# Kernel optimization log

Hardware: AMD Instinct MI355X
Metric: run time of the kernel (lower is better)

Reference implementation:

```python
import jax, jax.numpy as jnp
import numpy as np

B, C, H, W = 8, 512, 56, 56
CI = C // 2  # inter_channels
EPS = 1e-5   # BatchNorm eps


def setup_inputs() -> dict:
    key = jax.random.key(0)
    ks = jax.random.split(key, 11)
    s = 0.02
    return {
        "x": jax.random.normal(ks[0], (B, C, H, W), jnp.float32),
        "theta_w": jax.random.normal(ks[1], (CI, C), jnp.float32) * s,
        "theta_b": jnp.zeros((CI,), jnp.float32),
        "phi_w": jax.random.normal(ks[2], (CI, C), jnp.float32) * s,
        "phi_b": jnp.zeros((CI,), jnp.float32),
        "g_w": jax.random.normal(ks[3], (CI, C), jnp.float32) * s,
        "g_b": jnp.zeros((CI,), jnp.float32),
        "w_w": jax.random.normal(ks[4], (C, CI), jnp.float32) * s,
        "w_b": jnp.zeros((C,), jnp.float32),
        "bn_gamma": jax.random.normal(ks[5], (C,), jnp.float32) * 0.1,
        "bn_beta": jax.random.normal(ks[6], (C,), jnp.float32) * 0.1,
    }


def reference(x, theta_w, theta_b, phi_w, phi_b, g_w, g_b, w_w, w_b, bn_gamma, bn_beta):
    b, c, h, w = x.shape
    n = h * w

    def proj(wt, bi):  # 1x1 conv -> [b, out, n]
        return (jnp.einsum('bchw,oc->bohw', x, wt) + bi[None, :, None, None]).reshape(b, -1, n)

    theta_x = proj(theta_w, theta_b).transpose(0, 2, 1)  # [b, n, ci]
    phi_x = proj(phi_w, phi_b)                           # [b, ci, n]
    g_x = proj(g_w, g_b).transpose(0, 2, 1)             # [b, n, ci]

    f = jnp.einsum('bnc,bcm->bnm', theta_x, phi_x)       # [b, n, n] unscaled scores
    f_div_c = jax.nn.softmax(f, axis=-1)
    y = jnp.einsum('bnm,bmc->bnc', f_div_c, g_x)         # [b, n, ci]
    y = y.transpose(0, 2, 1).reshape(b, -1, h, w)        # [b, ci, h, w]

    w_y = jnp.einsum('bchw,oc->bohw', y, w_w) + w_b[None, :, None, None]
    # BatchNorm2d (training mode, batch statistics over B,H,W per channel)
    mean = w_y.mean(axis=(0, 2, 3))
    var = w_y.var(axis=(0, 2, 3))
    w_y = (w_y - mean[None, :, None, None]) * jax.lax.rsqrt(var[None, :, None, None] + EPS)
    w_y = w_y * bn_gamma[None, :, None, None] + bn_beta[None, :, None, None]
    return w_y + x
```

## Files before the change

kernel.cpp:

```cpp
#include <hip/hip_runtime.h>
#include <hip/hip_bf16.h>


typedef unsigned short u16;
typedef unsigned int u32;
typedef __attribute__((ext_vector_type(8))) short short8;
typedef __attribute__((ext_vector_type(4))) float floatx4;

#define B_   8
#define C_   512
#define CI_  256
#define N_   3136
#define BN_  25088

__device__ __forceinline__ u16 f2b(float f) {
    return __builtin_bit_cast(u16, __float2bfloat16(f));
}
__device__ __forceinline__ float b2f(u16 u) {
    return __bfloat162float(__builtin_bit_cast(__hip_bfloat16, u));
}
__device__ __forceinline__ floatx4 mfma16(short8 a, short8 b, floatx4 c) {
    return __builtin_amdgcn_mfma_f32_16x16x32_bf16(a, b, c, 0, 0, 0);
}
__device__ __forceinline__ void gload_lds16(const u16* g, u16* l) {
    __builtin_amdgcn_global_load_lds(
        (const __attribute__((address_space(1))) u32*)g,
        (__attribute__((address_space(3))) u32*)l, 16, 0, 0);
}

__global__ void detect_dtype(const u32* __restrict__ xw, int* __restrict__ flag)
{
    __shared__ int cnt;
    if (threadIdx.x == 0) cnt = 0;
    __syncthreads();
    int c = 0;
    for (int i = 0; i < 16; ++i) {
        u32 w = xw[threadIdx.x * 16 + i];
        u32 e = (w >> 7) & 0xFF;
        c += (e >= 118 && e <= 130) ? 1 : 0;
    }
    atomicAdd(&cnt, c);
    __syncthreads();
    if (threadIdx.x == 0) *flag = (2 * cnt > 4096) ? 1 : 0;
}

__global__ __launch_bounds__(256) void convert_params(
    const void* tw, const void* tb, const void* pw, const void* pb,
    const void* gw, const void* gbi, const void* ww, const void* wb,
    const void* gamma, const void* beta,
    u16* __restrict__ dst, const int* __restrict__ flag)
{
    const void* srcs[10] = {tw, tb, pw, pb, gw, gbi, ww, wb, gamma, beta};
    const int ns[10] = {131072, 256, 131072, 256, 131072, 256, 131072, 512, 512, 512};
    int seg = blockIdx.y;
    int off = 0;
    for (int s = 0; s < 10; ++s) { if (s == seg) break; off += ns[s]; }
    const void* src = srcs[seg];
    int n = ns[seg];
    int i0 = (blockIdx.x * 256 + threadIdx.x) * 8;
    if (i0 >= n) return;
    const int fl = *flag;
    u16* d = dst + off;
    for (int k = 0; k < 8; ++k) {
        int i = i0 + k;
        if (i < n)
            d[i] = fl ? ((const u16*)src)[i] : f2b(((const float*)src)[i]);
    }
}

__global__ __launch_bounds__(256) void transpose_x(
    const void* __restrict__ in, u16* __restrict__ out,
    const int* __restrict__ flag)
{
    __shared__ u16 tile[64][68];
    const int fl = *flag;
    const int t = threadIdx.x;
    const long base = (long)blockIdx.z * (long)C_ * (long)N_;
    const int c0 = blockIdx.x * 64, r0 = blockIdx.y * 64;
    const int lr = t >> 3;
    const int lc = (t & 7) * 8;
#pragma unroll
    for (int j = 0; j < 2; ++j) {
        int rr = lr + 32 * j;
        long eoff = base + (long)(r0 + rr) * N_ + c0 + lc;
        u16 v[8] __attribute__((aligned(16)));
        if (fl) {
            const u16* pi = (const u16*)in + eoff;
            *(uint64_t*)&v[0] = *(const uint64_t*)pi;
            *(uint64_t*)&v[4] = *(const uint64_t*)(pi + 4);
        } else {
            const float* pi = (const float*)in + eoff;
            floatx4 a = *(const floatx4*)pi;
            floatx4 b4 = *(const floatx4*)(pi + 4);
#pragma unroll
            for (int k = 0; k < 4; ++k) { v[k] = f2b(a[k]); v[4 + k] = f2b(b4[k]); }
        }
        *(uint64_t*)&tile[rr][lc] = *(const uint64_t*)&v[0];
        *(uint64_t*)&tile[rr][lc + 4] = *(const uint64_t*)&v[4];
    }
    __syncthreads();
#pragma unroll
    for (int j = 0; j < 2; ++j) {
        int oc = lr + 32 * j;
        int ob = (t & 7) * 8;
        u16 vals[8] __attribute__((aligned(16)));
#pragma unroll
        for (int k = 0; k < 8; ++k) vals[k] = tile[ob + k][oc];
        u16* po = out + (long)blockIdx.z * N_ * C_ + (long)(c0 + oc) * C_ + r0 + ob;
        *(uint64_t*)po = *(const uint64_t*)vals;
        *(uint64_t*)(po + 4) = *(const uint64_t*)(vals + 4);
    }
}

__global__ __launch_bounds__(256) void transpose64(
    const u16* __restrict__ in, u16* __restrict__ out, int R, int Cc)
{
    __shared__ u16 tile[64][68];
    const int t = threadIdx.x;
    const long base = (long)blockIdx.z * (long)R * (long)Cc;
    const int c0 = blockIdx.x * 64, r0 = blockIdx.y * 64;
    const int lr = t >> 3;
    const int lc = (t & 7) * 8;
#pragma unroll
    for (int j = 0; j < 2; ++j) {
        int rr = lr + 32 * j;
        const u16* pi = in + base + (long)(r0 + rr) * Cc + c0 + lc;
        *(uint64_t*)&tile[rr][lc] = *(const uint64_t*)pi;
        *(uint64_t*)&tile[rr][lc + 4] = *(const uint64_t*)(pi + 4);
    }
    __syncthreads();
#pragma unroll
    for (int j = 0; j < 2; ++j) {
        int oc = lr + 32 * j;
        int ob = (t & 7) * 8;
        u16 vals[8] __attribute__((aligned(16)));
#pragma unroll
        for (int k = 0; k < 8; ++k) vals[k] = tile[ob + k][oc];
        u16* po = out + base + (long)(c0 + oc) * R + r0 + ob;
        *(uint64_t*)po = *(const uint64_t*)vals;
        *(uint64_t*)(po + 4) = *(const uint64_t*)(vals + 4);
    }
}

template<int K>
__global__ __launch_bounds__(256) void gemm_bt(
    const u16* __restrict__ A, long a_bstride,
    const u16* __restrict__ Bt,
    const u16* __restrict__ bias,
    u16* __restrict__ Out, long out_bstride,
    int ncols)
{
    const int t = threadIdx.x;
    const int wave = t >> 6, lane = t & 63;
    const int q = lane >> 4, lx = lane & 15;
    const int m0 = blockIdx.x * 64;
    const int n0c = blockIdx.y * 64;
    const int b = blockIdx.z;
    const u16* Ab = A + (long)b * a_bstride;

    __shared__ u16 As[64][40];
    __shared__ u16 Bs[64][40];

    floatx4 zero4 = {0.f, 0.f, 0.f, 0.f};
    floatx4 acc[2][2];
#pragma unroll
    for (int i = 0; i < 2; ++i)
#pragma unroll
        for (int j = 0; j < 2; ++j) acc[i][j] = zero4;

    const int sr = t >> 2;
    const int sc = (t & 3) * 8;
    const int wr = (wave >> 1) * 32;
    const int wc = (wave & 1) * 32;

    for (int k0 = 0; k0 < K; k0 += 32) {
        *(short8*)&As[sr][sc] =
            *(const short8*)(Ab + (long)(m0 + sr) * K + k0 + sc);
        *(short8*)&Bs[sr][sc] =
            *(const short8*)(Bt + (long)(n0c + sr) * K + k0 + sc);
        __syncthreads();
        short8 af[2], bfr[2];
#pragma unroll
        for (int i = 0; i < 2; ++i)
            af[i] = *(const short8*)&As[wr + 16 * i + lx][q * 8];
#pragma unroll
        for (int j = 0; j < 2; ++j)
            bfr[j] = *(const short8*)&Bs[wc + 16 * j + lx][q * 8];
#pragma unroll
        for (int i = 0; i < 2; ++i)
#pragma unroll
            for (int j = 0; j < 2; ++j)
                acc[i][j] = mfma16(af[i], bfr[j], acc[i][j]);
        __syncthreads();
    }

#pragma unroll
    for (int i = 0; i < 2; ++i) {
#pragma unroll
        for (int j = 0; j < 2; ++j) {
            int col = n0c + wc + 16 * j + lx;
            float bv = b2f(bias[col]);
#pragma unroll
            for (int r = 0; r < 4; ++r) {
                int row = m0 + wr + 16 * i + q * 4 + r;
                Out[(long)b * out_bstride + (long)row * ncols + col] =
                    f2b(acc[i][j][r] + bv);
            }
        }
    }
}

__global__ __launch_bounds__(256, 2) void attn(
    const u16* __restrict__ theta,
    const u16* __restrict__ phi,
    const u16* __restrict__ gT,
    u16* __restrict__ ypart,
    float* __restrict__ lpart)
{
    __shared__ u16 ps[2][8][32][32];
    __shared__ u16 gs[2][256][32];
    __shared__ u16 Ps[4][32][40];

    const int t = threadIdx.x;
    const int wave = t >> 6, lane = t & 63;
    const int q = lane >> 4, lx = lane & 15;
    const int b = blockIdx.y;
    const int z = blockIdx.z;
    const int n0w = blockIdx.x * 128 + wave * 32;
    const bool valid = n0w < N_;
    const u16* thb = theta + (long)b * N_ * CI_;
    const u16* phb = phi + (long)b * N_ * CI_;
    const u16* gb = gT + (long)b * CI_ * N_;

    short8 tf[2][8];
#pragma unroll
    for (int h = 0; h < 2; ++h) {
        int trow = n0w + h * 16 + lx;
        if (trow >= N_) trow = N_ - 1;
#pragma unroll
        for (int kk = 0; kk < 8; ++kk)
            tf[h][kk] = *(const short8*)(thb + (long)trow * CI_ + kk * 32 + q * 8);
    }

    floatx4 zero4 = {0.f, 0.f, 0.f, 0.f};
    floatx4 yacc[2][16];
#pragma unroll
    for (int h = 0; h < 2; ++h)
#pragma unroll
        for (int i = 0; i < 16; ++i) yacc[h][i] = zero4;
    floatx4 lacc[2] = {zero4, zero4};
    const short8 ones = {0x3F80, 0x3F80, 0x3F80, 0x3F80,
                         0x3F80, 0x3F80, 0x3F80, 0x3F80};

    const int mbeg = z * (N_ / 2);
    const int lrow = lane >> 2;
    const int lcol = (lane & 3) * 8;

    auto stage = [&](int buf, int m0) {
#pragma unroll
        for (int i = 0; i < 2; ++i) {
            int kc = wave * 2 + i;
#pragma unroll
            for (int h = 0; h < 2; ++h)
                gload_lds16(phb + (long)(m0 + h * 16 + lrow) * CI_ + kc * 32 + lcol,
                            &ps[buf][kc][h * 16][0]);
        }
#pragma unroll
        for (int j4 = 0; j4 < 4; ++j4) {
            int j = wave * 4 + j4;
            gload_lds16(gb + (long)(j * 16 + lrow) * N_ + m0 + lcol,
                        &gs[buf][j * 16][0]);
        }
    };

    stage(0, mbeg);
    const int NSTEP = (N_ / 2) / 32;
    for (int s = 0; s < NSTEP; ++s) {
        const int buf = s & 1;
        __syncthreads();
        if (s + 1 < NSTEP) stage(buf ^ 1, mbeg + (s + 1) * 32);

        floatx4 sacc[2][2];
        sacc[0][0] = zero4; sacc[0][1] = zero4;
        sacc[1][0] = zero4; sacc[1][1] = zero4;
#pragma unroll
        for (int kk = 0; kk < 8; ++kk) {
            short8 bf0 = *(const short8*)&ps[buf][kk][lx][q * 8];
            short8 bf1 = *(const short8*)&ps[buf][kk][16 + lx][q * 8];
            sacc[0][0] = mfma16(tf[0][kk], bf0, sacc[0][0]);
            sacc[1][0] = mfma16(tf[1][kk], bf0, sacc[1][0]);
            sacc[0][1] = mfma16(tf[0][kk], bf1, sacc[0][1]);
            sacc[1][1] = mfma16(tf[1][kk], bf1, sacc[1][1]);
        }

#pragma unroll
        for (int h = 0; h < 2; ++h)
#pragma unroll
            for (int mh = 0; mh < 2; ++mh)
#pragma unroll
                for (int r = 0; r < 4; ++r) {
                    float e = __expf(fminf(sacc[h][mh][r], 60.f));
                    Ps[wave][h * 16 + q * 4 + r][mh * 16 + lx] = f2b(e);
                }
        __builtin_amdgcn_wave_barrier();
        short8 pA0 = *(const short8*)&Ps[wave][lx][q * 8];
        short8 pA1 = *(const short8*)&Ps[wave][16 + lx][q * 8];
        __builtin_amdgcn_wave_barrier();

#pragma unroll
        for (int ct = 0; ct < 16; ++ct) {
            short8 gf = *(const short8*)&gs[buf][ct * 16 + lx][q * 8];
            yacc[0][ct] = mfma16(pA0, gf, yacc[0][ct]);
            yacc[1][ct] = mfma16(pA1, gf, yacc[1][ct]);
        }
        lacc[0] = mfma16(pA0, ones, lacc[0]);
        lacc[1] = mfma16(pA1, ones, lacc[1]);
    }

    if (valid) {
        u16* yb = ypart + (long)z * B_ * N_ * CI_ + (long)b * N_ * CI_;
#pragma unroll
        for (int h = 0; h < 2; ++h)
#pragma unroll
            for (int ct = 0; ct < 16; ++ct)
#pragma unroll
                for (int r = 0; r < 4; ++r)
                    yb[(long)(n0w + h * 16 + q * 4 + r) * CI_ + ct * 16 + lx] =
                        f2b(yacc[h][ct][r]);
        if (lx == 0) {
#pragma unroll
            for (int h = 0; h < 2; ++h)
#pragma unroll
                for (int r = 0; r < 4; ++r)
                    lpart[(long)z * BN_ + (long)b * N_ + n0w + h * 16 + q * 4 + r] =
                        lacc[h][r];
        }
    }
}

__global__ __launch_bounds__(256) void attn_combine(
    const u16* __restrict__ ypart, const float* __restrict__ lpart,
    u16* __restrict__ y)
{
    long tt = (long)blockIdx.x * 256 + threadIdx.x;
    long row = tt >> 5;
    int cb = (int)(tt & 31) * 8;
    float l = lpart[row] + lpart[BN_ + row];
    float rl = 1.0f / l;
    const u16* p0 = ypart + row * CI_ + cb;
    const u16* p1 = p0 + (long)B_ * N_ * CI_;
    short8 v0 = *(const short8*)p0;
    short8 v1 = *(const short8*)p1;
    u16 ov[8] __attribute__((aligned(16)));
#pragma unroll
    for (int j = 0; j < 8; ++j)
        ov[j] = f2b((b2f(((const u16*)&v0)[j]) + b2f(((const u16*)&v1)[j])) * rl);
    *(short8*)(y + row * CI_ + cb) = *(const short8*)ov;
}

__global__ void zero_stats(float* stats) {
    stats[threadIdx.x] = 0.f;
    stats[threadIdx.x + 256] = 0.f;
    stats[threadIdx.x + 512] = 0.f;
    stats[threadIdx.x + 768] = 0.f;
}

__global__ __launch_bounds__(256) void bn_stats(
    const u16* __restrict__ wy, float* __restrict__ stats)
{
    const int t = threadIdx.x;
    const long row0 = (long)blockIdx.x * 256;
    float s0 = 0.f, s1 = 0.f, q0 = 0.f, q1 = 0.f;
    for (int r = 0; r < 256; ++r) {
        const u16* p = wy + (row0 + r) * C_;
        float a = b2f(p[t]), b = b2f(p[t + 256]);
        s0 += a; q0 += a * a;
        s1 += b; q1 += b * b;
    }
    atomicAdd(&stats[t], s0);
    atomicAdd(&stats[t + 256], s1);
    atomicAdd(&stats[C_ + t], q0);
    atomicAdd(&stats[C_ + t + 256], q1);
}

__global__ __launch_bounds__(256) void bn_apply(
    const u16* __restrict__ wy, const void* __restrict__ xv,
    const u16* __restrict__ gamma, const u16* __restrict__ beta,
    const float* __restrict__ stats, void* __restrict__ outv,
    const int* __restrict__ flag)
{
    __shared__ float tile[64][65];
    const int fl = *flag;
    const int t = threadIdx.x;
    const int nb0 = blockIdx.x * 64;
    const int c0 = blockIdx.y * 64;
    const int b = blockIdx.z;
#pragma unroll
    for (int j = 0; j < 4; ++j) {
        int row = (t >> 4) + 16 * j;
        int col = (t & 15) * 4;
        const u16* p = wy + ((long)b * N_ + nb0 + row) * C_ + c0 + col;
        u16 lv[4] __attribute__((aligned(8)));
        *(uint64_t*)lv = *(const uint64_t*)p;
#pragma unroll
        for (int k = 0; k < 4; ++k) tile[row][col + k] = b2f(lv[k]);
    }
    __syncthreads();
    const float inv = 1.0f / (float)BN_;
#pragma unroll
    for (int it = 0; it < 8; ++it) {
        int oc = (t >> 5) + 8 * it;
        int on = (t & 31) * 2;
        int c = c0 + oc;
        float mean = stats[c] * inv;
        float var = stats[C_ + c] * inv - mean * mean;
        float rstd = rsqrtf(var + 1e-5f);
        float sc = b2f(gamma[c]) * rstd;
        float sh = b2f(beta[c]) - mean * sc;
        long base = ((long)b * C_ + c) * N_ + nb0 + on;
        float v0 = tile[on][oc] * sc + sh;
        float v1 = tile[on + 1][oc] * sc + sh;
        if (fl) {
            v0 += b2f(((const u16*)xv)[base]);
            v1 += b2f(((const u16*)xv)[base + 1]);
            ((u16*)outv)[base] = f2b(v0);
            ((u16*)outv)[base + 1] = f2b(v1);
        } else {
            v0 += ((const float*)xv)[base];
            v1 += ((const float*)xv)[base + 1];
            ((float*)outv)[base] = v0;
            ((float*)outv)[base + 1] = v1;
        }
    }
}

extern "C" void kernel_launch(void* const* d_in, const int* in_sizes, int n_in,
                              void* d_out, int out_size, void* d_ws, size_t ws_size,
                              hipStream_t stream)
{
    (void)in_sizes; (void)n_in; (void)out_size; (void)ws_size;

    const size_t S = 12845056;
    char* base = (char*)d_ws;
    u16*   xT    = (u16*)(base);
    u16*   gT    = (u16*)(base);
    u16*   y     = (u16*)(base + S);
    u16*   th    = (u16*)(base + 2 * S);
    u16*   ph    = (u16*)(base + 3 * S);
    u16*   wy    = (u16*)(base + 2 * S);
    u16*   gn    = (u16*)(base + 4 * S);
    float* lpart = (float*)(base + 5 * S);
    float* stats = (float*)(base + 5 * S + (size_t)2 * BN_ * 4);
    u16*   cw    = (u16*)(base + 5 * S + (size_t)2 * BN_ * 4 + 4096);
    int*   flag  = (int*)(base + 5 * S + (size_t)2 * BN_ * 4 + 4096 + 1055744);

    u16* ctw = cw;               u16* ctb = cw + 131072;
    u16* cpw = ctb + 256;        u16* cpb = cpw + 131072;
    u16* cgw = cpb + 256;        u16* cgb = cgw + 131072;
    u16* cww = cgb + 256;        u16* cwb = cww + 131072;
    u16* cga = cwb + 512;        u16* cbe = cga + 512;

    u16* ypart = (u16*)d_out;

    detect_dtype<<<1, 256, 0, stream>>>((const u32*)d_in[0], flag);
    convert_params<<<dim3(64, 10), 256, 0, stream>>>(
        d_in[1], d_in[2], d_in[3], d_in[4], d_in[5], d_in[6], d_in[7],
        d_in[8], d_in[9], d_in[10], cw, flag);

    transpose_x<<<dim3(N_ / 64, C_ / 64, B_), 256, 0, stream>>>(d_in[0], xT, flag);

    gemm_bt<C_><<<dim3(N_ / 64, CI_ / 64, B_), 256, 0, stream>>>(
        xT, (long)N_ * C_, ctw, ctb, th, (long)N_ * CI_, CI_);
    gemm_bt<C_><<<dim3(N_ / 64, CI_ / 64, B_), 256, 0, stream>>>(
        xT, (long)N_ * C_, cpw, cpb, ph, (long)N_ * CI_, CI_);
    gemm_bt<C_><<<dim3(N_ / 64, CI_ / 64, B_), 256, 0, stream>>>(
        xT, (long)N_ * C_, cgw, cgb, gn, (long)N_ * CI_, CI_);

    transpose64<<<dim3(CI_ / 64, N_ / 64, B_), 256, 0, stream>>>(gn, gT, N_, CI_);

    attn<<<dim3(25, B_, 2), 256, 0, stream>>>(th, ph, gT, ypart, lpart);

    attn_combine<<<dim3((BN_ * 32) / 256), 256, 0, stream>>>(ypart, lpart, y);

    gemm_bt<CI_><<<dim3(N_ / 64, C_ / 64, B_), 256, 0, stream>>>(
        y, (long)N_ * CI_, cww, cwb, wy, (long)N_ * C_, C_);

    zero_stats<<<1, 256, 0, stream>>>(stats);
    bn_stats<<<BN_ / 256, 256, 0, stream>>>(wy, stats);

    bn_apply<<<dim3(N_ / 64, C_ / 64, B_), 256, 0, stream>>>(
        wy, d_in[0], cga, cbe, stats, d_out, flag);
}
```

Before: 392.0 us.

## Use fragment-ordered LDS layouts and double-buffered async loads in GEMM and attention

Measured after the change: 428.8 us. 1.09x slower.

```diff
diff --git a/kernel.cpp b/kernel.cpp
--- a/kernel.cpp
+++ b/kernel.cpp
@@ -143,13 +143,16 @@
 }
 
 template<int K>
-__global__ __launch_bounds__(256) void gemm_bt(
+__global__ __launch_bounds__(256, 4) void gemm_bt(
     const u16* __restrict__ A, long a_bstride,
     const u16* __restrict__ Bt,
     const u16* __restrict__ bias,
     u16* __restrict__ Out, long out_bstride,
     int ncols)
 {
+    __shared__ __attribute__((aligned(16))) u16 Asf[2][2][4][64][8];
+    __shared__ __attribute__((aligned(16))) u16 Bsf[2][2][4][64][8];
+
     const int t = threadIdx.x;
     const int wave = t >> 6, lane = t & 63;
     const int q = lane >> 4, lx = lane & 15;
@@ -158,9 +161,6 @@
     const int b = blockIdx.z;
     const u16* Ab = A + (long)b * a_bstride;
 
-    __shared__ u16 As[64][40];
-    __shared__ u16 Bs[64][40];
-
     floatx4 zero4 = {0.f, 0.f, 0.f, 0.f};
     floatx4 acc[2][2];
 #pragma unroll
@@ -168,32 +168,37 @@
 #pragma unroll
         for (int j = 0; j < 2; ++j) acc[i][j] = zero4;
 
-    const int sr = t >> 2;
-    const int sc = (t & 3) * 8;
-    const int wr = (wave >> 1) * 32;
-    const int wc = (wave & 1) * 32;
-
-    for (int k0 = 0; k0 < K; k0 += 32) {
-        *(short8*)&As[sr][sc] =
-            *(const short8*)(Ab + (long)(m0 + sr) * K + k0 + sc);
-        *(short8*)&Bs[sr][sc] =
-            *(const short8*)(Bt + (long)(n0c + sr) * K + k0 + sc);
+    auto stage = [&](int buf, int k0) {
+#pragma unroll
+        for (int ks = 0; ks < 2; ++ks) {
+            gload_lds16(Ab + (long)(m0 + wave * 16 + lx) * K + k0 + ks * 32 + q * 8,
+                        &Asf[buf][ks][wave][0][0]);
+            gload_lds16(Bt + (long)(n0c + wave * 16 + lx) * K + k0 + ks * 32 + q * 8,
+                        &Bsf[buf][ks][wave][0][0]);
+        }
+    };
+
+    stage(0, 0);
+    const int rg = (wave >> 1) * 2, cg = (wave & 1) * 2;
+    const int NS = K / 64;
+    for (int s = 0; s < NS; ++s) {
+        const int buf = s & 1;
         __syncthreads();
-        short8 af[2], bfr[2];
-#pragma unroll
-        for (int i = 0; i < 2; ++i)
-            af[i] = *(const short8*)&As[wr + 16 * i + lx][q * 8];
-#pragma unroll
-        for (int j = 0; j < 2; ++j)
-            bfr[j] = *(const short8*)&Bs[wc + 16 * j + lx][q * 8];
-#pragma unroll
-        for (int i = 0; i < 2; ++i)
-#pragma unroll
-            for (int j = 0; j < 2; ++j)
-                acc[i][j] = mfma16(af[i], bfr[j], acc[i][j]);
-        __syncthreads();
-    }
-
+        if (s + 1 < NS) stage(buf ^ 1, (s + 1) * 64);
+#pragma unroll
+        for (int ks = 0; ks < 2; ++ks) {
+            short8 af0 = *(const short8*)&Asf[buf][ks][rg][lane][0];
+            short8 af1 = *(const short8*)&Asf[buf][ks][rg + 1][lane][0];
+            short8 bf0 = *(const short8*)&Bsf[buf][ks][cg][lane][0];
+            short8 bf1 = *(const short8*)&Bsf[buf][ks][cg + 1][lane][0];
+            acc[0][0] = mfma16(af0, bf0, acc[0][0]);
+            acc[0][1] = mfma16(af0, bf1, acc[0][1]);
+            acc[1][0] = mfma16(af1, bf0, acc[1][0]);
+            acc[1][1] = mfma16(af1, bf1, acc[1][1]);
+        }
+    }
+
+    const int wr = (wave >> 1) * 32, wc = (wave & 1) * 32;
 #pragma unroll
     for (int i = 0; i < 2; ++i) {
 #pragma unroll
@@ -217,9 +222,9 @@
     u16* __restrict__ ypart,
     float* __restrict__ lpart)
 {
-    __shared__ u16 ps[2][8][32][32];
-    __shared__ u16 gs[2][256][32];
-    __shared__ u16 Ps[4][32][40];
+    __shared__ __attribute__((aligned(16))) u16 psf[2][8][2][64][8];
+    __shared__ __attribute__((aligned(16))) u16 gsf[2][16][64][8];
+    __shared__ __attribute__((aligned(16))) u16 Ps[4][32][40];
 
     const int t = threadIdx.x;
     const int wave = t >> 6, lane = t & 63;
@@ -253,8 +258,6 @@
                          0x3F80, 0x3F80, 0x3F80, 0x3F80};
 
     const int mbeg = z * (N_ / 2);
-    const int lrow = lane >> 2;
-    const int lcol = (lane & 3) * 8;
 
     auto stage = [&](int buf, int m0) {
 #pragma unroll
@@ -262,14 +265,14 @@
             int kc = wave * 2 + i;
 #pragma unroll
             for (int h = 0; h < 2; ++h)
-                gload_lds16(phb + (long)(m0 + h * 16 + lrow) * CI_ + kc * 32 + lcol,
-                            &ps[buf][kc][h * 16][0]);
+                gload_lds16(phb + (long)(m0 + h * 16 + lx) * CI_ + kc * 32 + q * 8,
+                            &psf[buf][kc][h][0][0]);
         }
 #pragma unroll
         for (int j4 = 0; j4 < 4; ++j4) {
-            int j = wave * 4 + j4;
-            gload_lds16(gb + (long)(j * 16 + lrow) * N_ + m0 + lcol,
-                        &gs[buf][j * 16][0]);
+            int ct = wave * 4 + j4;
+            gload_lds16(gb + (long)(ct * 16 + lx) * N_ + m0 + q * 8,
+                        &gsf[buf][ct][0][0]);
         }
     };
 
@@ -285,8 +288,8 @@
         sacc[1][0] = zero4; sacc[1][1] = zero4;
 #pragma unroll
         for (int kk = 0; kk < 8; ++kk) {
-            short8 bf0 = *(const short8*)&ps[buf][kk][lx][q * 8];
-            short8 bf1 = *(const short8*)&ps[buf][kk][16 + lx][q * 8];
+            short8 bf0 = *(const short8*)&psf[buf][kk][0][lane][0];
+            short8 bf1 = *(const short8*)&psf[buf][kk][1][lane][0];
             sacc[0][0] = mfma16(tf[0][kk], bf0, sacc[0][0]);
             sacc[1][0] = mfma16(tf[1][kk], bf0, sacc[1][0]);
             sacc[0][1] = mfma16(tf[0][kk], bf1, sacc[0][1]);
@@ -309,7 +312,7 @@
 
 #pragma unroll
         for (int ct = 0; ct < 16; ++ct) {
-            short8 gf = *(const short8*)&gs[buf][ct * 16 + lx][q * 8];
+            short8 gf = *(const short8*)&gsf[buf][ct][lane][0];
             yacc[0][ct] = mfma16(pA0, gf, yacc[0][ct]);
             yacc[1][ct] = mfma16(pA1, gf, yacc[1][ct]);
         }
```
